# Performance work log

Measured on AMD Instinct MI355X. Metric: run time of the kernel, lower is better.

The kernel has to match this reference:

```python
import jax, jax.numpy as jnp
import numpy as np


def setup_inputs() -> dict:
    key = jax.random.key(0)
    ks = jax.random.split(key, 9)
    N, L, E, H = 8, 4096, 1024, 16
    D = E // H
    return {
        "values": jax.random.normal(ks[0], (N, L, E), dtype=jnp.float32),
        "keys": jax.random.normal(ks[1], (N, L, E), dtype=jnp.float32),
        "query": jax.random.normal(ks[2], (N, L, E), dtype=jnp.float32),
        "mask": jax.random.randint(ks[3], (1, 1, H, H), 0, 2, dtype=jnp.int32),
        "Wv": jax.random.normal(ks[4], (D, D), dtype=jnp.float32) / np.sqrt(D),
        "Wk": jax.random.normal(ks[5], (D, D), dtype=jnp.float32) / np.sqrt(D),
        "Wq": jax.random.normal(ks[6], (D, D), dtype=jnp.float32) / np.sqrt(D),
        "Wo": jax.random.normal(ks[7], (E, E), dtype=jnp.float32) / np.sqrt(E),
        "bo": jnp.zeros((E,), dtype=jnp.float32),
    }


def reference(values, keys, query, mask, Wv, Wk, Wq, Wo, bo):
    N, L, E = query.shape
    H = mask.shape[-1]          # heads
    D = E // H                  # head_dim
    # reshape to (N, L, H, D) then per-head Dense(head_dim) on last dim
    v = values.reshape(N, L, H, D) @ Wv
    k = keys.reshape(N, L, H, D) @ Wk
    q = query.reshape(N, L, H, D) @ Wq
    # Faithful to the source: keys transposed with perm [0,1,3,2], so matmul
    # batches over (N, L) and energy is a (H x H) matrix per position.
    energy = jnp.einsum("nlhd,nlgd->nlhg", q, k)  # (N, L, H, H)
    energy = jnp.where(mask == 0, jnp.float32(-1e20), energy)
    attention = jax.nn.softmax(energy / (E ** 0.5), axis=-1)
    out = jnp.einsum("nlhg,nlgd->nlhd", attention, v)  # (N, L, H, D)
    # source: transpose to (N, H, L, D) then reshape to (N, L, H*D)
    out = out.transpose(0, 2, 1, 3).reshape(N, L, H * D)
    out = out @ Wo + bo
    return out, attention
```

## Files before the change

kernel.cpp:

```cpp
#include <hip/hip_runtime.h>

typedef short short8 __attribute__((ext_vector_type(8)));
typedef unsigned uint2v __attribute__((ext_vector_type(2)));
typedef float f32x4 __attribute__((ext_vector_type(4)));
typedef unsigned short u16;

#define MFMA16(a, b, c) __builtin_amdgcn_mfma_f32_16x16x32_bf16(a, b, c, 0, 0, 0)
#define GLD_LDS(g, l)                                                          \
  __builtin_amdgcn_global_load_lds(                                            \
      (__attribute__((address_space(1))) void*)(void*)(g),                     \
      (__attribute__((address_space(3))) void*)(l), 16, 0, 0)

__device__ __forceinline__ u16 f2bf(float f) {
  union { float f; unsigned u; } x; x.f = f;
  unsigned r = x.u + 0x7fffu + ((x.u >> 16) & 1u);
  return (u16)(r >> 16);
}

__device__ __forceinline__ unsigned pk2(float a, float b) {
  return (unsigned)f2bf(a) | ((unsigned)f2bf(b) << 16);
}
__device__ __forceinline__ uint2v pk4(f32x4 a) {
  uint2v r;
  r[0] = pk2(a[0], a[1]);
  r[1] = pk2(a[2], a[3]);
  return r;
}

__global__ __launch_bounds__(256) void prep(const float* __restrict__ Wv,
                                            const float* __restrict__ Wk,
                                            const float* __restrict__ Wq,
                                            const float* __restrict__ Wo,
                                            u16* __restrict__ WoT2,
                                            u16* __restrict__ Mt) {
  __shared__ __align__(16) float A[64][65];
  __shared__ __align__(16) float B[64][68];
  const int t = threadIdx.x;
  const int r = t >> 2, c = (t & 3) * 16;
  if (blockIdx.x < 256) {
    const int tr = blockIdx.x >> 4, tc = blockIdx.x & 15;
#pragma unroll
    for (int u = 0; u < 4; ++u)
      *(float4*)&A[r][c + u * 4] = *(const float4*)(Wv + r * 64 + c + u * 4);
#pragma unroll
    for (int u = 0; u < 4; ++u)
      *(float4*)&B[r][c + u * 4] =
          *(const float4*)(Wo + (tr * 64 + r) * 1024 + tc * 64 + c + u * 4);
    __syncthreads();
    const int n = t & 63, i0 = (t >> 6) * 16;
    float acc[16];
#pragma unroll
    for (int ii = 0; ii < 16; ++ii) acc[ii] = 0.f;
    for (int j = 0; j < 64; ++j) {
      const float wo = B[j][n];
#pragma unroll
      for (int ii = 0; ii < 16; ++ii) acc[ii] += A[i0 + ii][j] * wo;
    }
    u16* dst = WoT2 + (size_t)(tc * 64 + n) * 1024 + tr * 64 + i0;
    short8 o0, o1;
#pragma unroll
    for (int jj = 0; jj < 8; ++jj) { o0[jj] = (short)f2bf(acc[jj]); o1[jj] = (short)f2bf(acc[8 + jj]); }
    *(short8*)(void*)dst = o0;
    *(short8*)(void*)(dst + 8) = o1;
  } else {
#pragma unroll
    for (int u = 0; u < 4; ++u)
      *(float4*)&A[r][c + u * 4] = *(const float4*)(Wq + r * 64 + c + u * 4);
#pragma unroll
    for (int u = 0; u < 4; ++u)
      *(float4*)&B[r][c + u * 4] = *(const float4*)(Wk + r * 64 + c + u * 4);
    __syncthreads();
    const int n = t & 63, k0 = (t >> 6) * 16;
    float acc[16];
#pragma unroll
    for (int ii = 0; ii < 16; ++ii) acc[ii] = 0.f;
    for (int d = 0; d < 64; ++d) {
      const float wk = B[n][d];
#pragma unroll
      for (int kk = 0; kk < 16; ++kk) acc[kk] += A[k0 + kk][d] * wk;
    }
    u16* dst = Mt + n * 64 + k0;
    short8 o0, o1;
#pragma unroll
    for (int jj = 0; jj < 8; ++jj) { o0[jj] = (short)f2bf(acc[jj]); o1[jj] = (short)f2bf(acc[8 + jj]); }
    *(short8*)(void*)dst = o0;
    *(short8*)(void*)(dst + 8) = o1;
  }
}

__global__ __launch_bounds__(256, 4) void attn_kernel(
    const float* __restrict__ values, const float* __restrict__ keys,
    const float* __restrict__ query, const int* __restrict__ mask,
    const u16* __restrict__ Mt, float* __restrict__ attn,
    u16* __restrict__ out2) {
  __shared__ __align__(16) u16 x1[4][16][68];
  __shared__ __align__(16) u16 x2[4][16][68];
  __shared__ __align__(16) u16 vTp[4][64][24];

  const int tid = threadIdx.x;
  const int w = tid >> 6, lane = tid & 63;
  const int g16 = lane & 15;
  const int q4 = lane >> 4;
  const int kbase = q4 * 8;
  const int mrow = q4 * 4;
  const int pg16 = (g16 & 3) * 4 + (g16 >> 2);

  u16 (*mt)[68] = (u16(*)[68]) & x1[0][0][0];
  {
    const short8* mg = (const short8*)Mt;
    short8 a0 = mg[tid];
    short8 a1 = mg[256 + tid];
    *(short8*)&mt[tid >> 3][(tid & 7) * 8] = a0;
    const int g1 = 256 + tid;
    *(short8*)&mt[g1 >> 3][(g1 & 7) * 8] = a1;
  }
  __syncthreads();
  short8 mtf[2][4];
#pragma unroll
  for (int kb = 0; kb < 2; ++kb)
#pragma unroll
    for (int nc = 0; nc < 4; ++nc)
      mtf[kb][nc] = *(const short8*)&mt[nc * 16 + g16][kb * 32 + kbase];
  __syncthreads();

  int mzb = 0;
#pragma unroll
  for (int r = 0; r < 4; ++r)
    mzb |= (mask[(mrow + r) * 16 + g16] == 0) ? (1 << r) : 0;

  const f32x4 zero = {0.f, 0.f, 0.f, 0.f};
  const int pbase = blockIdx.x * 16 + w * 4;

  const f32x4* qv = (const f32x4*)query;
  const f32x4* kv = (const f32x4*)keys;
  const f32x4* vv = (const f32x4*)values;
  const size_t b0 = (size_t)pbase * 256 + lane;

  f32x4 qf0 = qv[b0], qf1 = qv[b0 + 64], qf2 = qv[b0 + 128], qf3 = qv[b0 + 192];
  f32x4 kf0 = kv[b0], kf1 = kv[b0 + 64], kf2 = kv[b0 + 128], kf3 = kv[b0 + 192];
  f32x4 vf0 = vv[b0], vf1 = vv[b0 + 64], vf2 = vv[b0 + 128], vf3 = vv[b0 + 192];

  const int wr = lane >> 4;
  const int wc = (lane & 15) * 4;

#pragma unroll
  for (int i = 0; i < 4; ++i) {
    const int p = pbase + i;

    *(uint2v*)&x1[w][0 + wr][wc] = pk4(qf0);
    *(uint2v*)&x1[w][4 + wr][wc] = pk4(qf1);
    *(uint2v*)&x1[w][8 + wr][wc] = pk4(qf2);
    *(uint2v*)&x1[w][12 + wr][wc] = pk4(qf3);
    *(uint2v*)&x2[w][0 + wr][wc] = pk4(kf0);
    *(uint2v*)&x2[w][4 + wr][wc] = pk4(kf1);
    *(uint2v*)&x2[w][8 + wr][wc] = pk4(kf2);
    *(uint2v*)&x2[w][12 + wr][wc] = pk4(kf3);
#pragma unroll
    for (int j = 0; j < 4; ++j) {
      uint2v col;
      col[0] = pk2(vf0[j], vf1[j]);
      col[1] = pk2(vf2[j], vf3[j]);
      *(uint2v*)&vTp[w][wc + j][wr * 4] = col;
    }

    if (i < 3) {
      const size_t nb = b0 + (size_t)(i + 1) * 256;
      qf0 = qv[nb]; qf1 = qv[nb + 64]; qf2 = qv[nb + 128]; qf3 = qv[nb + 192];
      kf0 = kv[nb]; kf1 = kv[nb + 64]; kf2 = kv[nb + 128]; kf3 = kv[nb + 192];
      vf0 = vv[nb]; vf1 = vv[nb + 64]; vf2 = vv[nb + 128]; vf3 = vv[nb + 192];
    }
    __builtin_amdgcn_sched_barrier(0);

    short8 aq0 = *(const short8*)&x1[w][g16][kbase];
    short8 aq1 = *(const short8*)&x1[w][g16][32 + kbase];
    short8 ak0 = *(const short8*)&x2[w][g16][kbase];
    short8 ak1 = *(const short8*)&x2[w][g16][32 + kbase];

    f32x4 tacc[4];
#pragma unroll
    for (int nc = 0; nc < 4; ++nc) {
      tacc[nc] = MFMA16(aq0, mtf[0][nc], zero);
      tacc[nc] = MFMA16(aq1, mtf[1][nc], tacc[nc]);
    }
#pragma unroll
    for (int nc = 0; nc < 4; ++nc)
#pragma unroll
      for (int r = 0; r < 4; ++r)
        x1[w][mrow + r][nc * 16 + g16] = f2bf(tacc[nc][r]);

    short8 ea0 = *(const short8*)&x1[w][g16][kbase];
    short8 ea1 = *(const short8*)&x1[w][g16][32 + kbase];
    f32x4 acce = MFMA16(ea0, ak0, zero);
    acce = MFMA16(ea1, ak1, acce);

    const float SC = 0.045084220027780106f;
    float* ap = attn + (size_t)p * 256 + mrow * 16 + g16;
#pragma unroll
    for (int r = 0; r < 4; ++r) {
      const float val = ((mzb >> r) & 1) ? -45.f : acce[r] * SC;
      const float pe = exp2f(val);
      float s = pe;
      s += __shfl_xor(s, 1, 16);
      s += __shfl_xor(s, 2, 16);
      s += __shfl_xor(s, 4, 16);
      s += __shfl_xor(s, 8, 16);
      const float a = pe * __builtin_amdgcn_rcpf(s);
      ap[r * 16] = a;
      x2[w][mrow + r][pg16] = f2bf(a);
    }

    short8 pa;
    if (lane < 32) {
      pa = *(const short8*)&x2[w][g16][kbase];
    } else {
      short8 z = {0, 0, 0, 0, 0, 0, 0, 0};
      pa = z;
    }
    const int gsel = (lane < 32) ? kbase : 0;
#pragma unroll
    for (int nc = 0; nc < 4; ++nc) {
      short8 vb = *(const short8*)&vTp[w][nc * 16 + g16][gsel];
      f32x4 acco = MFMA16(pa, vb, zero);
#pragma unroll
      for (int r = 0; r < 4; ++r)
        x1[w][mrow + r][nc * 16 + g16] = f2bf(acco[r]);
    }

    {
      short8 s0 = *(const short8*)&x1[w][lane >> 3][(lane & 7) * 8];
      short8 s1 = *(const short8*)&x1[w][8 + (lane >> 3)][(lane & 7) * 8];
      u16* dst = out2 + (size_t)p * 1024 + lane * 8;
      *(short8*)(void*)dst = s0;
      *(short8*)(void*)(dst + 512) = s1;
    }
  }
}

__global__ __launch_bounds__(256, 2) void gemm_kernel(
    const u16* __restrict__ A, const u16* __restrict__ BT,
    const float* __restrict__ bo, float* __restrict__ C) {
  __shared__ __align__(16) u16 As[128 * 32];
  __shared__ __align__(16) u16 Bs[128 * 32];
  const int t = threadIdx.x, lane = t & 63;
  const int g16 = lane & 15, q4 = lane >> 4;
  const int w = t >> 6, wm = w >> 1, wn = w & 1;
  const int bm = blockIdx.x & 255, bn = blockIdx.x >> 8;

  f32x4 acc[4][4];
  const f32x4 zero = {0.f, 0.f, 0.f, 0.f};
#pragma unroll
  for (int mt = 0; mt < 4; ++mt)
#pragma unroll
    for (int nt = 0; nt < 4; ++nt) acc[mt][nt] = zero;

  const int am = t >> 2, ak = (t & 3) * 8;
  const int R0 = bm * 128 + am;
  const int R1 = R0 + 64;
  const size_t base0 =
      ((size_t)((R0 >> 12) * 4096 + (R0 & 255) * 16)) * 1024 +
      ((R0 & 4095) >> 8) * 64;
  const size_t base1 =
      ((size_t)((R1 >> 12) * 4096 + (R1 & 255) * 16)) * 1024 +
      ((R1 & 4095) >> 8) * 64;
  const u16* ga0 = A + base0 + ak;
  const u16* ga1 = A + base1 + ak;
  const u16* gb = BT + (size_t)(bn * 128 + am) * 1024 + ak;
  u16* lA = &As[t * 8];
  u16* lB = &Bs[t * 8];

  for (int kt = 0; kt < 32; ++kt) {
    __syncthreads();
    const int aoff = (kt >> 1) * 1024 + (kt & 1) * 32;
    const int ko = kt * 32;
    GLD_LDS(ga0 + aoff, lA);
    GLD_LDS(ga1 + aoff, lA + 2048);
    GLD_LDS(gb + ko, lB);
    GLD_LDS(gb + 64 * 1024 + ko, lB + 2048);
    __syncthreads();

    short8 af[4], bf[4];
#pragma unroll
    for (int mt = 0; mt < 4; ++mt)
      af[mt] = *(const short8*)&As[(wm * 64 + mt * 16 + g16) * 32 + q4 * 8];
#pragma unroll
    for (int nt = 0; nt < 4; ++nt)
      bf[nt] = *(const short8*)&Bs[(wn * 64 + nt * 16 + g16) * 32 + q4 * 8];
#pragma unroll
    for (int mt = 0; mt < 4; ++mt)
#pragma unroll
      for (int nt = 0; nt < 4; ++nt)
        acc[mt][nt] = MFMA16(af[mt], bf[nt], acc[mt][nt]);
  }

#pragma unroll
  for (int nt = 0; nt < 4; ++nt) {
    const int col = bn * 128 + wn * 64 + nt * 16 + g16;
    const float bias = bo[col];
#pragma unroll
    for (int mt = 0; mt < 4; ++mt) {
#pragma unroll
      for (int r = 0; r < 4; ++r) {
        const int row = bm * 128 + wm * 64 + mt * 16 + q4 * 4 + r;
        C[(size_t)row * 1024 + col] = acc[mt][nt][r] + bias;
      }
    }
  }
}

extern "C" void kernel_launch(void* const* d_in, const int* in_sizes, int n_in,
                              void* d_out, int out_size, void* d_ws,
                              size_t ws_size, hipStream_t stream) {
  const float* values = (const float*)d_in[0];
  const float* keys   = (const float*)d_in[1];
  const float* query  = (const float*)d_in[2];
  const int*   mask   = (const int*)d_in[3];
  const float* Wv = (const float*)d_in[4];
  const float* Wk = (const float*)d_in[5];
  const float* Wq = (const float*)d_in[6];
  const float* Wo = (const float*)d_in[7];
  const float* bo = (const float*)d_in[8];

  float* out  = (float*)d_out;
  float* attn = out + 33554432;

  u16* out2 = (u16*)d_ws;
  u16* WoT2 = out2 + 33554432;
  u16* Mt   = WoT2 + 1048576;

  prep<<<257, 256, 0, stream>>>(Wv, Wk, Wq, Wo, WoT2, Mt);
  attn_kernel<<<2048, 256, 0, stream>>>(values, keys, query, mask, Mt, attn,
                                        out2);
  gemm_kernel<<<2048, 256, 0, stream>>>(out2, WoT2, bo, out);
}
```

Before: 236.8 us.

## Stage QKV loads via async global-to-LDS double buffering in persistent waves

The attention kernel now loads query/keys/values rows with global_load_lds into a per-wave double-buffered fp32 LDS staging area, prefetching the next position while computing the current one. Each wave processes 16 positions instead of 4, with the grid cut from 2048 to 512 blocks and the occupancy hint removed. The aim is to keep more memory traffic in flight and drop the register-held prefetch. The cost is a much larger LDS footprint, about 96KB of staging per block, which limits residency to one or two blocks per CU and leaves fewer blocks to hide latency.

```diff
diff --git a/kernel.cpp b/kernel.cpp
--- a/kernel.cpp
+++ b/kernel.cpp
@@ -8,7 +8,7 @@
 #define MFMA16(a, b, c) __builtin_amdgcn_mfma_f32_16x16x32_bf16(a, b, c, 0, 0, 0)
 #define GLD_LDS(g, l)                                                          \
   __builtin_amdgcn_global_load_lds(                                            \
-      (__attribute__((address_space(1))) void*)(void*)(g),                     \
+      (__attribute__((address_space(1))) const void*)(const void*)(g),         \
       (__attribute__((address_space(3))) void*)(l), 16, 0, 0)
 
 __device__ __forceinline__ u16 f2bf(float f) {
@@ -16,14 +16,15 @@
   unsigned r = x.u + 0x7fffu + ((x.u >> 16) & 1u);
   return (u16)(r >> 16);
 }
-
 __device__ __forceinline__ unsigned pk2(float a, float b) {
   return (unsigned)f2bf(a) | ((unsigned)f2bf(b) << 16);
 }
-__device__ __forceinline__ uint2v pk4(f32x4 a) {
-  uint2v r;
-  r[0] = pk2(a[0], a[1]);
-  r[1] = pk2(a[2], a[3]);
+__device__ __forceinline__ short8 pack8(f32x4 a, f32x4 b) {
+  short8 r;
+  r[0] = (short)f2bf(a[0]); r[1] = (short)f2bf(a[1]);
+  r[2] = (short)f2bf(a[2]); r[3] = (short)f2bf(a[3]);
+  r[4] = (short)f2bf(b[0]); r[5] = (short)f2bf(b[1]);
+  r[6] = (short)f2bf(b[2]); r[7] = (short)f2bf(b[3]);
   return r;
 }
 
@@ -88,11 +89,12 @@
   }
 }
 
-__global__ __launch_bounds__(256, 4) void attn_kernel(
+__global__ __launch_bounds__(256) void attn_kernel(
     const float* __restrict__ values, const float* __restrict__ keys,
     const float* __restrict__ query, const int* __restrict__ mask,
     const u16* __restrict__ Mt, float* __restrict__ attn,
     u16* __restrict__ out2) {
+  __shared__ __align__(16) float stg[4][2][3][1024];
   __shared__ __align__(16) u16 x1[4][16][68];
   __shared__ __align__(16) u16 x2[4][16][68];
   __shared__ __align__(16) u16 vTp[4][64][24];
@@ -104,23 +106,25 @@
   const int kbase = q4 * 8;
   const int mrow = q4 * 4;
   const int pg16 = (g16 & 3) * 4 + (g16 >> 2);
-
-  u16 (*mt)[68] = (u16(*)[68]) & x1[0][0][0];
+  const int wr = lane >> 4;
+  const int wc = (lane & 15) * 4;
+
   {
-    const short8* mg = (const short8*)Mt;
-    short8 a0 = mg[tid];
-    short8 a1 = mg[256 + tid];
-    *(short8*)&mt[tid >> 3][(tid & 7) * 8] = a0;
-    const int g1 = 256 + tid;
-    *(short8*)&mt[g1 >> 3][(g1 & 7) * 8] = a1;
+    u16* mtl = (u16*)&stg[0][0][0][0];
+    ((short8*)mtl)[tid] = ((const short8*)Mt)[tid];
+    ((short8*)mtl)[256 + tid] = ((const short8*)Mt)[256 + tid];
   }
   __syncthreads();
   short8 mtf[2][4];
-#pragma unroll
-  for (int kb = 0; kb < 2; ++kb)
-#pragma unroll
-    for (int nc = 0; nc < 4; ++nc)
-      mtf[kb][nc] = *(const short8*)&mt[nc * 16 + g16][kb * 32 + kbase];
+  {
+    const u16* mtl = (const u16*)&stg[0][0][0][0];
+#pragma unroll
+    for (int kb = 0; kb < 2; ++kb)
+#pragma unroll
+      for (int nc = 0; nc < 4; ++nc)
+        mtf[kb][nc] =
+            *(const short8*)&mtl[(nc * 16 + g16) * 64 + kb * 32 + kbase];
+  }
   __syncthreads();
 
   int mzb = 0;
@@ -129,52 +133,67 @@
     mzb |= (mask[(mrow + r) * 16 + g16] == 0) ? (1 << r) : 0;
 
   const f32x4 zero = {0.f, 0.f, 0.f, 0.f};
-  const int pbase = blockIdx.x * 16 + w * 4;
-
-  const f32x4* qv = (const f32x4*)query;
-  const f32x4* kv = (const f32x4*)keys;
-  const f32x4* vv = (const f32x4*)values;
-  const size_t b0 = (size_t)pbase * 256 + lane;
-
-  f32x4 qf0 = qv[b0], qf1 = qv[b0 + 64], qf2 = qv[b0 + 128], qf3 = qv[b0 + 192];
-  f32x4 kf0 = kv[b0], kf1 = kv[b0 + 64], kf2 = kv[b0 + 128], kf3 = kv[b0 + 192];
-  f32x4 vf0 = vv[b0], vf1 = vv[b0 + 64], vf2 = vv[b0 + 128], vf3 = vv[b0 + 192];
-
-  const int wr = lane >> 4;
-  const int wc = (lane & 15) * 4;
-
-#pragma unroll
-  for (int i = 0; i < 4; ++i) {
-    const int p = pbase + i;
-
-    *(uint2v*)&x1[w][0 + wr][wc] = pk4(qf0);
-    *(uint2v*)&x1[w][4 + wr][wc] = pk4(qf1);
-    *(uint2v*)&x1[w][8 + wr][wc] = pk4(qf2);
-    *(uint2v*)&x1[w][12 + wr][wc] = pk4(qf3);
-    *(uint2v*)&x2[w][0 + wr][wc] = pk4(kf0);
-    *(uint2v*)&x2[w][4 + wr][wc] = pk4(kf1);
-    *(uint2v*)&x2[w][8 + wr][wc] = pk4(kf2);
-    *(uint2v*)&x2[w][12 + wr][wc] = pk4(kf3);
-#pragma unroll
-    for (int j = 0; j < 4; ++j) {
-      uint2v col;
-      col[0] = pk2(vf0[j], vf1[j]);
-      col[1] = pk2(vf2[j], vf3[j]);
-      *(uint2v*)&vTp[w][wc + j][wr * 4] = col;
-    }
-
-    if (i < 3) {
-      const size_t nb = b0 + (size_t)(i + 1) * 256;
-      qf0 = qv[nb]; qf1 = qv[nb + 64]; qf2 = qv[nb + 128]; qf3 = qv[nb + 192];
-      kf0 = kv[nb]; kf1 = kv[nb + 64]; kf2 = kv[nb + 128]; kf3 = kv[nb + 192];
-      vf0 = vv[nb]; vf1 = vv[nb + 64]; vf2 = vv[nb + 128]; vf3 = vv[nb + 192];
+  const int p0 = (blockIdx.x * 4 + w) * 16;
+
+#define STAGE(p, buf)                                                          \
+  {                                                                            \
+    const float* gq = query + (size_t)(p) * 1024 + (lane << 2);                \
+    const float* gk = keys + (size_t)(p) * 1024 + (lane << 2);                 \
+    const float* gv = values + (size_t)(p) * 1024 + (lane << 2);               \
+    float* dq = &stg[w][buf][0][lane << 2];                                    \
+    float* dk = &stg[w][buf][1][lane << 2];                                    \
+    float* dv = &stg[w][buf][2][lane << 2];                                    \
+    GLD_LDS(gq + 0, dq + 0);     GLD_LDS(gq + 256, dq + 256);                  \
+    GLD_LDS(gq + 512, dq + 512); GLD_LDS(gq + 768, dq + 768);                  \
+    GLD_LDS(gk + 0, dk + 0);     GLD_LDS(gk + 256, dk + 256);                  \
+    GLD_LDS(gk + 512, dk + 512); GLD_LDS(gk + 768, dk + 768);                  \
+    GLD_LDS(gv + 0, dv + 0);     GLD_LDS(gv + 256, dv + 256);                  \
+    GLD_LDS(gv + 512, dv + 512); GLD_LDS(gv + 768, dv + 768);                  \
+  }
+
+  STAGE(p0, 0);
+
+#pragma unroll 1
+  for (int i = 0; i < 16; ++i) {
+    const int p = p0 + i;
+    const int cur = i & 1;
+
+    if (i < 15) {
+      STAGE(p + 1, cur ^ 1);
+      asm volatile("s_waitcnt vmcnt(12)" ::: "memory");
+    } else {
+      asm volatile("s_waitcnt vmcnt(0)" ::: "memory");
     }
     __builtin_amdgcn_sched_barrier(0);
 
-    short8 aq0 = *(const short8*)&x1[w][g16][kbase];
-    short8 aq1 = *(const short8*)&x1[w][g16][32 + kbase];
-    short8 ak0 = *(const short8*)&x2[w][g16][kbase];
-    short8 ak1 = *(const short8*)&x2[w][g16][32 + kbase];
+    const float* sq = &stg[w][cur][0][0];
+    const float* sk = &stg[w][cur][1][0];
+    const float* sv = &stg[w][cur][2][0];
+
+    f32x4 qa0 = *(const f32x4*)&sq[g16 * 64 + kbase];
+    f32x4 qa1 = *(const f32x4*)&sq[g16 * 64 + kbase + 4];
+    f32x4 qb0 = *(const f32x4*)&sq[g16 * 64 + 32 + kbase];
+    f32x4 qb1 = *(const f32x4*)&sq[g16 * 64 + 32 + kbase + 4];
+    f32x4 ka0 = *(const f32x4*)&sk[g16 * 64 + kbase];
+    f32x4 ka1 = *(const f32x4*)&sk[g16 * 64 + kbase + 4];
+    f32x4 kb0 = *(const f32x4*)&sk[g16 * 64 + 32 + kbase];
+    f32x4 kb1 = *(const f32x4*)&sk[g16 * 64 + 32 + kbase + 4];
+    short8 aq0 = pack8(qa0, qa1), aq1 = pack8(qb0, qb1);
+    short8 ak0 = pack8(ka0, ka1), ak1 = pack8(kb0, kb1);
+
+    {
+      f32x4 vf0 = *(const f32x4*)&sv[(0 + wr) * 64 + wc];
+      f32x4 vf1 = *(const f32x4*)&sv[(4 + wr) * 64 + wc];
+      f32x4 vf2 = *(const f32x4*)&sv[(8 + wr) * 64 + wc];
+      f32x4 vf3 = *(const f32x4*)&sv[(12 + wr) * 64 + wc];
+#pragma unroll
+      for (int j = 0; j < 4; ++j) {
+        uint2v col;
+        col[0] = pk2(vf0[j], vf1[j]);
+        col[1] = pk2(vf2[j], vf3[j]);
+        *(uint2v*)&vTp[w][wc + j][wr * 4] = col;
+      }
+    }
 
     f32x4 tacc[4];
 #pragma unroll
@@ -234,6 +253,7 @@
       *(short8*)(void*)(dst + 512) = s1;
     }
   }
+#undef STAGE
 }
 
 __global__ __launch_bounds__(256, 2) void gemm_kernel(
@@ -328,7 +348,7 @@
   u16* Mt   = WoT2 + 1048576;
 
   prep<<<257, 256, 0, stream>>>(Wv, Wk, Wq, Wo, WoT2, Mt);
-  attn_kernel<<<2048, 256, 0, stream>>>(values, keys, query, mask, Mt, attn,
-                                        out2);
+  attn_kernel<<<512, 256, 0, stream>>>(values, keys, query, mask, Mt, attn,
+                                       out2);
   gemm_kernel<<<2048, 256, 0, stream>>>(out2, WoT2, bo, out);
 }
```

After: 247.8 us. 4.6% more time.

## Rewrite output GEMM with 8-wave 128x256 tiles, triple-buffered LDS and swizzle

Applied to the files above, without the earlier changes.

Replaces the 4-wave 128x128 GEMM, which had a single LDS buffer and two syncs per 32-wide K step, with an 8-wave 128x256-tile kernel that uses 64-wide K steps. Tiles are loaded into a 3-stage LDS ring through direct global-to-LDS loads. Prefetch is issued two stages ahead, interleaved with split MFMA phases and setprio, and the LDS layout is XOR-swizzled to avoid bank conflicts. The goal is to hide memory latency and raise MFMA utilization. In exchange, the kernel uses much more LDS (about 144KB per block), which limits occupancy.

```diff
diff --git a/kernel.cpp b/kernel.cpp
--- a/kernel.cpp
+++ b/kernel.cpp
@@ -8,7 +8,7 @@
 #define MFMA16(a, b, c) __builtin_amdgcn_mfma_f32_16x16x32_bf16(a, b, c, 0, 0, 0)
 #define GLD_LDS(g, l)                                                          \
   __builtin_amdgcn_global_load_lds(                                            \
-      (__attribute__((address_space(1))) void*)(void*)(g),                     \
+      (__attribute__((address_space(1))) const void*)(const void*)(g),         \
       (__attribute__((address_space(3))) void*)(l), 16, 0, 0)
 
 __device__ __forceinline__ u16 f2bf(float f) {
@@ -16,15 +16,8 @@
   unsigned r = x.u + 0x7fffu + ((x.u >> 16) & 1u);
   return (u16)(r >> 16);
 }
-
 __device__ __forceinline__ unsigned pk2(float a, float b) {
   return (unsigned)f2bf(a) | ((unsigned)f2bf(b) << 16);
-}
-__device__ __forceinline__ uint2v pk4(f32x4 a) {
-  uint2v r;
-  r[0] = pk2(a[0], a[1]);
-  r[1] = pk2(a[2], a[3]);
-  return r;
 }
 
 __global__ __launch_bounds__(256) void prep(const float* __restrict__ Wv,
@@ -147,14 +140,14 @@
   for (int i = 0; i < 4; ++i) {
     const int p = pbase + i;
 
-    *(uint2v*)&x1[w][0 + wr][wc] = pk4(qf0);
-    *(uint2v*)&x1[w][4 + wr][wc] = pk4(qf1);
-    *(uint2v*)&x1[w][8 + wr][wc] = pk4(qf2);
-    *(uint2v*)&x1[w][12 + wr][wc] = pk4(qf3);
-    *(uint2v*)&x2[w][0 + wr][wc] = pk4(kf0);
-    *(uint2v*)&x2[w][4 + wr][wc] = pk4(kf1);
-    *(uint2v*)&x2[w][8 + wr][wc] = pk4(kf2);
-    *(uint2v*)&x2[w][12 + wr][wc] = pk4(kf3);
+    *(uint2v*)&x1[w][0 + wr][wc] = uint2v{pk2(qf0[0], qf0[1]), pk2(qf0[2], qf0[3])};
+    *(uint2v*)&x1[w][4 + wr][wc] = uint2v{pk2(qf1[0], qf1[1]), pk2(qf1[2], qf1[3])};
+    *(uint2v*)&x1[w][8 + wr][wc] = uint2v{pk2(qf2[0], qf2[1]), pk2(qf2[2], qf2[3])};
+    *(uint2v*)&x1[w][12 + wr][wc] = uint2v{pk2(qf3[0], qf3[1]), pk2(qf3[2], qf3[3])};
+    *(uint2v*)&x2[w][0 + wr][wc] = uint2v{pk2(kf0[0], kf0[1]), pk2(kf0[2], kf0[3])};
+    *(uint2v*)&x2[w][4 + wr][wc] = uint2v{pk2(kf1[0], kf1[1]), pk2(kf1[2], kf1[3])};
+    *(uint2v*)&x2[w][8 + wr][wc] = uint2v{pk2(kf2[0], kf2[1]), pk2(kf2[2], kf2[3])};
+    *(uint2v*)&x2[w][12 + wr][wc] = uint2v{pk2(kf3[0], kf3[1]), pk2(kf3[2], kf3[3])};
 #pragma unroll
     for (int j = 0; j < 4; ++j) {
       uint2v col;
@@ -236,72 +229,137 @@
   }
 }
 
-__global__ __launch_bounds__(256, 2) void gemm_kernel(
+__global__ __launch_bounds__(512, 2) void gemm8_kernel(
     const u16* __restrict__ A, const u16* __restrict__ BT,
     const float* __restrict__ bo, float* __restrict__ C) {
-  __shared__ __align__(16) u16 As[128 * 32];
-  __shared__ __align__(16) u16 Bs[128 * 32];
-  const int t = threadIdx.x, lane = t & 63;
+  __shared__ __align__(16) u16 As[3][128 * 64];
+  __shared__ __align__(16) u16 Bs[3][256 * 64];
+  const int tid = threadIdx.x;
+  const int lane = tid & 63;
+  const int w = tid >> 6;
+  const int wm = w >> 2, wn = w & 3;
   const int g16 = lane & 15, q4 = lane >> 4;
-  const int w = t >> 6, wm = w >> 1, wn = w & 1;
-  const int bm = blockIdx.x & 255, bn = blockIdx.x >> 8;
+  const int bm = blockIdx.x >> 2, bn = blockIdx.x & 3;
+
+  const int r0 = tid >> 3, sl = tid & 7;
+  const int r1 = r0 + 64;
+  const int sw0 = sl ^ (r0 & 7);
+  const int sw1 = sl ^ (r1 & 7);
+  const int R0 = bm * 128 + r0, R1 = bm * 128 + r1;
+  const size_t a_src0 =
+      ((size_t)((R0 >> 12) * 4096 + (R0 & 255) * 16)) * 1024 +
+      ((R0 & 4095) >> 8) * 64 + sw0 * 8;
+  const size_t a_src1 =
+      ((size_t)((R1 >> 12) * 4096 + (R1 & 255) * 16)) * 1024 +
+      ((R1 & 4095) >> 8) * 64 + sw1 * 8;
+  const size_t b_src00 = (size_t)(bn * 256 + r0) * 1024 + sw0 * 8;
+  const size_t b_src01 = (size_t)(bn * 256 + r1) * 1024 + sw1 * 8;
+  const size_t b_src10 = (size_t)(bn * 256 + 128 + r0) * 1024 + sw0 * 8;
+  const size_t b_src11 = (size_t)(bn * 256 + 128 + r1) * 1024 + sw1 * 8;
+
+#define SA(kt, s)                                                              \
+  {                                                                            \
+    GLD_LDS(A + a_src0 + (kt) * 1024, &As[s][tid * 8]);                        \
+    GLD_LDS(A + a_src1 + (kt) * 1024, &As[s][tid * 8 + 4096]);                 \
+  }
+#define SB0(kt, s)                                                             \
+  {                                                                            \
+    GLD_LDS(BT + b_src00 + (kt) * 64, &Bs[s][tid * 8]);                        \
+    GLD_LDS(BT + b_src01 + (kt) * 64, &Bs[s][tid * 8 + 4096]);                 \
+  }
+#define SB1(kt, s)                                                             \
+  {                                                                            \
+    GLD_LDS(BT + b_src10 + (kt) * 64, &Bs[s][8192 + tid * 8]);                 \
+    GLD_LDS(BT + b_src11 + (kt) * 64, &Bs[s][8192 + tid * 8 + 4096]);          \
+  }
 
   f32x4 acc[4][4];
   const f32x4 zero = {0.f, 0.f, 0.f, 0.f};
 #pragma unroll
-  for (int mt = 0; mt < 4; ++mt)
-#pragma unroll
-    for (int nt = 0; nt < 4; ++nt) acc[mt][nt] = zero;
-
-  const int am = t >> 2, ak = (t & 3) * 8;
-  const int R0 = bm * 128 + am;
-  const int R1 = R0 + 64;
-  const size_t base0 =
-      ((size_t)((R0 >> 12) * 4096 + (R0 & 255) * 16)) * 1024 +
-      ((R0 & 4095) >> 8) * 64;
-  const size_t base1 =
-      ((size_t)((R1 >> 12) * 4096 + (R1 & 255) * 16)) * 1024 +
-      ((R1 & 4095) >> 8) * 64;
-  const u16* ga0 = A + base0 + ak;
-  const u16* ga1 = A + base1 + ak;
-  const u16* gb = BT + (size_t)(bn * 128 + am) * 1024 + ak;
-  u16* lA = &As[t * 8];
-  u16* lB = &Bs[t * 8];
-
-  for (int kt = 0; kt < 32; ++kt) {
-    __syncthreads();
-    const int aoff = (kt >> 1) * 1024 + (kt & 1) * 32;
-    const int ko = kt * 32;
-    GLD_LDS(ga0 + aoff, lA);
-    GLD_LDS(ga1 + aoff, lA + 2048);
-    GLD_LDS(gb + ko, lB);
-    GLD_LDS(gb + 64 * 1024 + ko, lB + 2048);
-    __syncthreads();
-
-    short8 af[4], bf[4];
-#pragma unroll
-    for (int mt = 0; mt < 4; ++mt)
-      af[mt] = *(const short8*)&As[(wm * 64 + mt * 16 + g16) * 32 + q4 * 8];
-#pragma unroll
-    for (int nt = 0; nt < 4; ++nt)
-      bf[nt] = *(const short8*)&Bs[(wn * 64 + nt * 16 + g16) * 32 + q4 * 8];
-#pragma unroll
-    for (int mt = 0; mt < 4; ++mt)
-#pragma unroll
-      for (int nt = 0; nt < 4; ++nt)
-        acc[mt][nt] = MFMA16(af[mt], bf[nt], acc[mt][nt]);
-  }
-
-#pragma unroll
-  for (int nt = 0; nt < 4; ++nt) {
-    const int col = bn * 128 + wn * 64 + nt * 16 + g16;
+  for (int m = 0; m < 4; ++m)
+#pragma unroll
+    for (int n = 0; n < 4; ++n) acc[m][n] = zero;
+
+  SA(0, 0); SB0(0, 0); SB1(0, 0);
+  SA(1, 1); SB0(1, 1); SB1(1, 1);
+  asm volatile("s_waitcnt vmcnt(6)" ::: "memory");
+  __builtin_amdgcn_sched_barrier(0);
+  __builtin_amdgcn_s_barrier();
+
+  const int swz = g16 & 7;
+  int rs = 0;
+#pragma unroll 1
+  for (int t = 0; t < 16; ++t) {
+    const int ss = (rs == 0) ? 2 : rs - 1;
+    const u16* Ar = &As[rs][0];
+    const u16* Br = &Bs[rs][0];
+
+    short8 af[4][2], bf[4][2];
+#pragma unroll
+    for (int m = 0; m < 4; ++m)
+#pragma unroll
+      for (int ks = 0; ks < 2; ++ks)
+        af[m][ks] = *(const short8*)&Ar[(wm * 64 + m * 16 + g16) * 64 +
+                                        (((ks << 2) + q4) ^ swz) * 8];
+#pragma unroll
+    for (int n = 0; n < 2; ++n)
+#pragma unroll
+      for (int ks = 0; ks < 2; ++ks)
+        bf[n][ks] = *(const short8*)&Br[(wn * 64 + n * 16 + g16) * 64 +
+                                        (((ks << 2) + q4) ^ swz) * 8];
+    if (t < 14) { SA(t + 2, ss); SB0(t + 2, ss); }
+    __builtin_amdgcn_s_barrier();
+    __builtin_amdgcn_s_setprio(1);
+#pragma unroll
+    for (int m = 0; m < 4; ++m)
+#pragma unroll
+      for (int n = 0; n < 2; ++n) {
+        acc[m][n] = MFMA16(af[m][0], bf[n][0], acc[m][n]);
+        acc[m][n] = MFMA16(af[m][1], bf[n][1], acc[m][n]);
+      }
+    __builtin_amdgcn_s_setprio(0);
+    __builtin_amdgcn_s_barrier();
+
+#pragma unroll
+    for (int n = 2; n < 4; ++n)
+#pragma unroll
+      for (int ks = 0; ks < 2; ++ks)
+        bf[n][ks] = *(const short8*)&Br[(wn * 64 + n * 16 + g16) * 64 +
+                                        (((ks << 2) + q4) ^ swz) * 8];
+    if (t < 14) SB1(t + 2, ss);
+    __builtin_amdgcn_s_barrier();
+    __builtin_amdgcn_s_setprio(1);
+#pragma unroll
+    for (int m = 0; m < 4; ++m)
+#pragma unroll
+      for (int n = 2; n < 4; ++n) {
+        acc[m][n] = MFMA16(af[m][0], bf[n][0], acc[m][n]);
+        acc[m][n] = MFMA16(af[m][1], bf[n][1], acc[m][n]);
+      }
+    __builtin_amdgcn_s_setprio(0);
+    if (t == 14) {
+      asm volatile("s_waitcnt vmcnt(0)" ::: "memory");
+    } else {
+      asm volatile("s_waitcnt vmcnt(6)" ::: "memory");
+    }
+    __builtin_amdgcn_sched_barrier(0);
+    __builtin_amdgcn_s_barrier();
+    rs = (rs == 2) ? 0 : rs + 1;
+  }
+#undef SA
+#undef SB0
+#undef SB1
+
+#pragma unroll
+  for (int n = 0; n < 4; ++n) {
+    const int col = bn * 256 + wn * 64 + n * 16 + g16;
     const float bias = bo[col];
 #pragma unroll
-    for (int mt = 0; mt < 4; ++mt) {
+    for (int m = 0; m < 4; ++m) {
 #pragma unroll
       for (int r = 0; r < 4; ++r) {
-        const int row = bm * 128 + wm * 64 + mt * 16 + q4 * 4 + r;
-        C[(size_t)row * 1024 + col] = acc[mt][nt][r] + bias;
+        const int row = bm * 128 + wm * 64 + m * 16 + q4 * 4 + r;
+        C[(size_t)row * 1024 + col] = acc[m][n][r] + bias;
       }
     }
   }
@@ -330,5 +388,5 @@
   prep<<<257, 256, 0, stream>>>(Wv, Wk, Wq, Wo, WoT2, Mt);
   attn_kernel<<<2048, 256, 0, stream>>>(values, keys, query, mask, Mt, attn,
                                         out2);
-  gemm_kernel<<<2048, 256, 0, stream>>>(out2, WoT2, bo, out);
-}
+  gemm8_kernel<<<1024, 512, 0, stream>>>(out2, WoT2, bo, out);
+}
```

New measurement: 229.7 us. -3.0%, faster.
